# Kernel tuning notes

Hardware: AMD Instinct MI355X
Metric: run time of the kernel (lower is better)

The kernel has to match this reference:

```python
import jax, jax.numpy as jnp
import numpy as np
import math

D_MODEL = 1024
LAYER_ID = 6
NUM_LAYERS = 12
B, T = 8, 2048
MIN_P = -1e38


def _init_params():
    C = D_MODEL
    r01 = LAYER_ID / (NUM_LAYERS - 1)
    r1a0 = 1.0 - LAYER_ID / NUM_LAYERS
    h = np.arange(C, dtype=np.float32)
    decay_speed = -5.0 + 8.0 * (h / (C - 1)) ** (0.7 + 1.3 * r01)
    zigzag = (((np.arange(C) + 1) % 3) - 1).astype(np.float32) * 0.5
    U = np.float32(math.log(0.3)) + zigzag
    xx = (np.arange(C, dtype=np.float32) / C).reshape(1, 1, C)
    tmk = xx ** r1a0
    tmv = xx ** r1a0 + 0.3 * r01
    tmr = xx ** (0.5 * r1a0)
    return (jnp.asarray(decay_speed), jnp.asarray(U), jnp.asarray(tmk, jnp.float32),
            jnp.asarray(tmv, jnp.float32), jnp.asarray(tmr, jnp.float32))


def setup_inputs() -> dict:
    key = jax.random.key(0)
    k0, k1, k2, k3, k4 = jax.random.split(key, 5)
    W, U, tmk, tmv, tmr = _init_params()
    C = D_MODEL
    s = 1.0 / math.sqrt(C)
    return {
        "x": jax.random.normal(k0, (B, T, C), jnp.float32),
        "W": W, "U": U,
        "time_mix_k": tmk, "time_mix_v": tmv, "time_mix_r": tmr,
        "Wk": jax.random.normal(k1, (C, C), jnp.float32) * s,
        "Wv": jax.random.normal(k2, (C, C), jnp.float32) * s,
        "Wr": jax.random.normal(k3, (C, C), jnp.float32) * s,
        "Wo": jax.random.normal(k4, (C, C), jnp.float32) * s,
    }


def _wkv(W, U, k, v):
    # W, U: [C]; k, v: [B, T, C]. Stable WKV recurrence with max-trick.
    w = -jnp.exp(W)  # negative decay, per channel
    Bb, Tt, Cc = k.shape
    aa0 = jnp.zeros((Bb, Cc), k.dtype)
    bb0 = jnp.zeros((Bb, Cc), k.dtype)
    pp0 = jnp.full((Bb, Cc), MIN_P, k.dtype)

    def step(carry, kv_t):
        aa, bb, pp = carry
        kt, vt = kv_t  # [B, C]
        ww = U + kt
        p = jnp.maximum(pp, ww)
        e1 = jnp.exp(pp - p)
        e2 = jnp.exp(ww - p)
        y = (e1 * aa + e2 * vt) / (e1 * bb + e2)
        ww2 = pp + w
        p2 = jnp.maximum(ww2, kt)
        e1b = jnp.exp(ww2 - p2)
        e2b = jnp.exp(kt - p2)
        return (e1b * aa + e2b * vt, e1b * bb + e2b, p2), y

    kT = jnp.swapaxes(k, 0, 1)  # [T, B, C]
    vT = jnp.swapaxes(v, 0, 1)
    _, yT = jax.lax.scan(step, (aa0, bb0, pp0), (kT, vT))
    return jnp.swapaxes(yT, 0, 1)  # [B, T, C]


def reference(x, W, U, time_mix_k, time_mix_v, time_mix_r, Wk, Wv, Wr, Wo):
    # token shift: prepend zero along T, drop last step
    xs = jnp.pad(x, ((0, 0), (1, 0), (0, 0)))[:, :-1]
    xk = x * time_mix_k + xs * (1.0 - time_mix_k)
    xv = x * time_mix_v + xs * (1.0 - time_mix_v)
    xr = x * time_mix_r + xs * (1.0 - time_mix_r)
    K = jnp.einsum('btc,dc->btd', xk, Wk)
    V = jnp.einsum('btc,dc->btd', xv, Wv)
    R = jnp.einsum('btc,dc->btd', xr, Wr)
    wkv = _wkv(W, U, K, V)
    hidden = jax.lax.stop_gradient(wkv[:, -1, :])
    rwkv = jax.nn.sigmoid(R) * wkv
    output = jnp.einsum('btc,dc->btd', rwkv, Wo)
    return output, hidden
```

## Files before the change

kernel.cpp:

```cpp
#include <hip/hip_runtime.h>

#define Bn 8
#define Tn 2048
#define Cn 1024
#define Mn (Bn * Tn)
#define LCH 64
#define NCH (Tn / LCH)

typedef __attribute__((ext_vector_type(8))) short short8;
typedef __attribute__((ext_vector_type(4))) float f32x4;

typedef const __attribute__((address_space(1))) void gas_void;
typedef __attribute__((address_space(3))) void las_void;

__device__ __forceinline__ unsigned short f2bf(float f) {
    unsigned int u = __float_as_uint(f);
    u += 0x7FFFu + ((u >> 16) & 1u);
    return (unsigned short)(u >> 16);
}
__device__ __forceinline__ float bf2f(unsigned short h) {
    return __uint_as_float(((unsigned int)h) << 16);
}

__global__ __launch_bounds__(256) void cvt_kernel(const float* __restrict__ src,
                                                  unsigned short* __restrict__ dst) {
    int i = blockIdx.x * 256 + threadIdx.x;
    float4 v = ((const float4*)src)[i];
    ushort4 o;
    o.x = f2bf(v.x); o.y = f2bf(v.y); o.z = f2bf(v.z); o.w = f2bf(v.w);
    ((ushort4*)dst)[i] = o;
}

__device__ __forceinline__ ushort4 mix4(const float4& a, const float4& s, const float4& m) {
    ushort4 o;
    o.x = f2bf(s.x + (a.x - s.x) * m.x);
    o.y = f2bf(s.y + (a.y - s.y) * m.y);
    o.z = f2bf(s.z + (a.z - s.z) * m.z);
    o.w = f2bf(s.w + (a.w - s.w) * m.w);
    return o;
}

__global__ __launch_bounds__(256) void mix_kernel(const float* __restrict__ x,
                                                  const float* __restrict__ tmk,
                                                  const float* __restrict__ tmv,
                                                  const float* __restrict__ tmr,
                                                  unsigned short* __restrict__ ak,
                                                  unsigned short* __restrict__ av,
                                                  unsigned short* __restrict__ ar) {
    int i = blockIdx.x * 256 + threadIdx.x;
    int c4 = i & 255;
    int t  = (i >> 8) & (Tn - 1);
    float4 xc = ((const float4*)x)[i];
    float4 xs = make_float4(0.f, 0.f, 0.f, 0.f);
    if (t > 0) xs = ((const float4*)x)[i - 256];
    float4 mk = ((const float4*)tmk)[c4];
    float4 mv = ((const float4*)tmv)[c4];
    float4 mr = ((const float4*)tmr)[c4];
    ((ushort4*)ak)[i] = mix4(xc, xs, mk);
    ((ushort4*)av)[i] = mix4(xc, xs, mv);
    ((ushort4*)ar)[i] = mix4(xc, xs, mr);
}

#define BK 32

template <int FOUT>
__global__ __launch_bounds__(256) void gemm_bt(const unsigned short* __restrict__ A,
                                               const unsigned short* __restrict__ Bw,
                                               unsigned short* __restrict__ Cb,
                                               float* __restrict__ Cf) {
    __shared__ unsigned short lA[128 * BK];
    __shared__ unsigned short lB[128 * BK];
    const int tid  = threadIdx.x;
    const int lane = tid & 63;
    const int wid  = tid >> 6;
    const int wr   = wid >> 1;
    const int wc   = wid & 1;
    const int bm   = blockIdx.x * 128;
    const int bn   = blockIdx.y * 128;

    const int srow = lane >> 2;
    const int scol = (lane & 3) * 8;
    const int lr   = lane & 15;
    const int lk   = (lane >> 4) * 8;

    f32x4 acc[4][4] = {};

    for (int k0 = 0; k0 < 1024; k0 += BK) {
#pragma unroll
        for (int i = 0; i < 2; ++i) {
            int r = wid * 32 + i * 16;
            const unsigned short* ga = A  + (size_t)(bm + r + srow) * 1024 + k0 + scol;
            const unsigned short* gb = Bw + (size_t)(bn + r + srow) * 1024 + k0 + scol;
            __builtin_amdgcn_global_load_lds((gas_void*)ga, (las_void*)&lA[r * BK], 16, 0, 0);
            __builtin_amdgcn_global_load_lds((gas_void*)gb, (las_void*)&lB[r * BK], 16, 0, 0);
        }
        __syncthreads();

        short8 af[4], bfv[4];
#pragma unroll
        for (int m = 0; m < 4; ++m)
            af[m] = *(const short8*)&lA[(wr * 64 + m * 16 + lr) * BK + lk];
#pragma unroll
        for (int n = 0; n < 4; ++n)
            bfv[n] = *(const short8*)&lB[(wc * 64 + n * 16 + lr) * BK + lk];
#pragma unroll
        for (int m = 0; m < 4; ++m)
#pragma unroll
            for (int n = 0; n < 4; ++n)
                acc[m][n] = __builtin_amdgcn_mfma_f32_16x16x32_bf16(af[m], bfv[n], acc[m][n], 0, 0, 0);
        __syncthreads();
    }

    const int crow0 = bm + wr * 64 + (lane >> 4) * 4;
    const int ccol0 = bn + wc * 64 + (lane & 15);
#pragma unroll
    for (int m = 0; m < 4; ++m) {
#pragma unroll
        for (int n = 0; n < 4; ++n) {
            int col = ccol0 + n * 16;
#pragma unroll
            for (int j = 0; j < 4; ++j) {
                size_t idx = (size_t)(crow0 + m * 16 + j) * 1024 + col;
                float v = acc[m][n][j];
                if (FOUT) Cf[idx] = v;
                else      Cb[idx] = f2bf(v);
            }
        }
    }
}

__global__ __launch_bounds__(256) void wkv_pass1(const unsigned short* __restrict__ K,
                                                 const unsigned short* __restrict__ V,
                                                 const float* __restrict__ Wd,
                                                 float* __restrict__ caa,
                                                 float* __restrict__ cbb,
                                                 float* __restrict__ cpp) {
    int c = blockIdx.x * 256 + threadIdx.x;
    int j = blockIdx.y;
    int b = blockIdx.z;
    float w = -__expf(Wd[c]);
    float aa = 0.f, bb = 0.f, pp = -1e38f;
    size_t base = ((size_t)(b * Tn + j * LCH)) * Cn + c;
#pragma unroll 4
    for (int t = 0; t < LCH; ++t) {
        size_t idx = base + (size_t)t * Cn;
        float kt = bf2f(K[idx]);
        float vt = bf2f(V[idx]);
        float ww2 = pp + w;
        float p2  = fmaxf(ww2, kt);
        float e1  = __expf(ww2 - p2);
        float e2  = __expf(kt - p2);
        aa = e1 * aa + e2 * vt;
        bb = e1 * bb + e2;
        pp = p2;
    }
    size_t o = ((size_t)b * NCH + j) * Cn + c;
    caa[o] = aa; cbb[o] = bb; cpp[o] = pp;
}

__global__ __launch_bounds__(256) void wkv_pass2(const float* __restrict__ Wd,
                                                 const float* __restrict__ caa,
                                                 const float* __restrict__ cbb,
                                                 const float* __restrict__ cpp,
                                                 float* __restrict__ saa,
                                                 float* __restrict__ sbb,
                                                 float* __restrict__ spp) {
    int c = blockIdx.x * 256 + threadIdx.x;
    int b = blockIdx.y;
    float Lw = -__expf(Wd[c]) * (float)LCH;
    float aa = 0.f, bb = 0.f, pp = -1e38f;
    for (int j = 0; j < NCH; ++j) {
        size_t o = ((size_t)b * NCH + j) * Cn + c;
        saa[o] = aa; sbb[o] = bb; spp[o] = pp;
        float qa = caa[o], qb = cbb[o], qp = cpp[o];
        float ppd = pp + Lw;
        float p  = fmaxf(ppd, qp);
        float e1 = __expf(ppd - p);
        float e2 = __expf(qp - p);
        aa = e1 * aa + e2 * qa;
        bb = e1 * bb + e2 * qb;
        pp = p;
    }
}

__global__ __launch_bounds__(256) void wkv_pass3(const unsigned short* __restrict__ K,
                                                 const unsigned short* __restrict__ V,
                                                 const unsigned short* __restrict__ Rb,
                                                 const float* __restrict__ Wd,
                                                 const float* __restrict__ Ud,
                                                 const float* __restrict__ saa,
                                                 const float* __restrict__ sbb,
                                                 const float* __restrict__ spp,
                                                 unsigned short* __restrict__ rwkv,
                                                 float* __restrict__ hidden) {
    int c = blockIdx.x * 256 + threadIdx.x;
    int j = blockIdx.y;
    int b = blockIdx.z;
    float w = -__expf(Wd[c]);
    float u = Ud[c];
    size_t o = ((size_t)b * NCH + j) * Cn + c;
    float aa = saa[o], bb = sbb[o], pp = spp[o];
    size_t base = ((size_t)(b * Tn + j * LCH)) * Cn + c;
    float y = 0.f;
#pragma unroll 4
    for (int t = 0; t < LCH; ++t) {
        size_t idx = base + (size_t)t * Cn;
        float kt = bf2f(K[idx]);
        float vt = bf2f(V[idx]);
        float rt = bf2f(Rb[idx]);
        float ww = u + kt;
        float p  = fmaxf(pp, ww);
        float e1 = __expf(pp - p);
        float e2 = __expf(ww - p);
        y = __fdividef(e1 * aa + e2 * vt, e1 * bb + e2);
        float sr = __fdividef(1.f, 1.f + __expf(-rt));
        rwkv[idx] = f2bf(sr * y);
        float ww2 = pp + w;
        float p2  = fmaxf(ww2, kt);
        float e1b = __expf(ww2 - p2);
        float e2b = __expf(kt - p2);
        aa = e1b * aa + e2b * vt;
        bb = e1b * bb + e2b;
        pp = p2;
    }
    if (j == NCH - 1) hidden[b * Cn + c] = y;
}

extern "C" void kernel_launch(void* const* d_in, const int* in_sizes, int n_in,
                              void* d_out, int out_size, void* d_ws, size_t ws_size,
                              hipStream_t stream) {
    const float* x   = (const float*)d_in[0];
    const float* Wd  = (const float*)d_in[1];
    const float* Ud  = (const float*)d_in[2];
    const float* tmk = (const float*)d_in[3];
    const float* tmv = (const float*)d_in[4];
    const float* tmr = (const float*)d_in[5];
    const float* Wk  = (const float*)d_in[6];
    const float* Wv  = (const float*)d_in[7];
    const float* Wr  = (const float*)d_in[8];
    const float* Wo  = (const float*)d_in[9];

    float* out    = (float*)d_out;
    float* hidden = out + (size_t)Mn * Cn;

    const size_t MK = (size_t)Mn * Cn;
    const size_t CC = (size_t)Cn * Cn;
    unsigned short* ak  = (unsigned short*)d_ws;
    unsigned short* av  = ak + MK;
    unsigned short* ar  = av + MK;
    unsigned short* Kb  = ar + MK;
    unsigned short* Wkb = Kb + MK;
    unsigned short* Wvb = Wkb + CC;
    unsigned short* Wrb = Wvb + CC;
    unsigned short* Wob = Wrb + CC;
    unsigned short* Vb = ak;
    unsigned short* Rb = av;
    unsigned short* rw = ar;
    const size_t SB = (size_t)Bn * NCH * Cn;
    float* caa = (float*)Wkb;
    float* cbb = caa + SB;
    float* cpp = cbb + SB;
    float* saa = cpp + SB;
    float* sbb = saa + SB;
    float* spp = sbb + SB;

    cvt_kernel<<<dim3(CC / 1024), 256, 0, stream>>>(Wk, Wkb);
    cvt_kernel<<<dim3(CC / 1024), 256, 0, stream>>>(Wv, Wvb);
    cvt_kernel<<<dim3(CC / 1024), 256, 0, stream>>>(Wr, Wrb);
    cvt_kernel<<<dim3(CC / 1024), 256, 0, stream>>>(Wo, Wob);

    mix_kernel<<<dim3(MK / 1024), 256, 0, stream>>>(x, tmk, tmv, tmr, ak, av, ar);

    dim3 gg(Mn / 128, Cn / 128);
    gemm_bt<0><<<gg, 256, 0, stream>>>(ak, Wkb, Kb, nullptr);
    gemm_bt<0><<<gg, 256, 0, stream>>>(av, Wvb, Vb, nullptr);
    gemm_bt<0><<<gg, 256, 0, stream>>>(ar, Wrb, Rb, nullptr);

    dim3 gw(Cn / 256, NCH, Bn);
    wkv_pass1<<<gw, 256, 0, stream>>>(Kb, Vb, Wd, caa, cbb, cpp);
    wkv_pass2<<<dim3(Cn / 256, Bn), 256, 0, stream>>>(Wd, caa, cbb, cpp, saa, sbb, spp);
    wkv_pass3<<<gw, 256, 0, stream>>>(Kb, Vb, Rb, Wd, Ud, saa, sbb, spp, rw, hidden);

    gemm_bt<1><<<gg, 256, 0, stream>>>(rw, Wob, nullptr, out);
}
```

Before: 408.4 us.

## Rewrite bf16 GEMM with 256x128 tiles, triple-buffered LDS and swizzled layout

Replaces the simple single-buffered 128x128 BK=32 GEMM with a 256x128 tile, 512-thread kernel that stages BK=64 slices into a three-deep LDS ring using async global_load_lds, XOR-swizzled rows and split phases with s_setprio around MFMA bursts. The goal is to overlap global loads with MFMA compute, cut LDS bank conflicts and raise reuse per loaded byte across the four GEMMs. It uses 144KB of LDS per block with hand-placed vmcnt waits and raw barriers, which limits occupancy and depends on exact counting of outstanding loads to stay correct.

```diff
diff --git a/kernel.cpp b/kernel.cpp
--- a/kernel.cpp
+++ b/kernel.cpp
@@ -61,67 +61,123 @@
     ((ushort4*)ar)[i] = mix4(xc, xs, mr);
 }
 
-#define BK 32
+
+#define NT 16
+#define BUFB 49152
+
+#define PHASE_BAR() asm volatile("s_barrier" ::: "memory")
+#define WAITV6()    asm volatile("s_waitcnt vmcnt(6)" ::: "memory")
+#define WAITV0()    asm volatile("s_waitcnt vmcnt(0)" ::: "memory")
+
+__device__ __forceinline__ void stage_rows(const unsigned short* gbase,
+                                           char* ldsbase, int lane, int wid) {
+    int rowg = wid * 16 + (lane >> 3);
+    int slot = (lane & 7) ^ (lane >> 3);
+    const unsigned short* s0 = gbase + (size_t)rowg * 1024 + slot * 8;
+    const unsigned short* s1 = gbase + (size_t)(rowg + 8) * 1024 + slot * 8;
+    char* d0 = ldsbase + (wid * 16) * 128;
+    char* d1 = ldsbase + (wid * 16 + 8) * 128;
+    __builtin_amdgcn_global_load_lds((gas_void*)s0, (las_void*)d0, 16, 0, 0);
+    __builtin_amdgcn_global_load_lds((gas_void*)s1, (las_void*)d1, 16, 0, 0);
+}
 
 template <int FOUT>
-__global__ __launch_bounds__(256) void gemm_bt(const unsigned short* __restrict__ A,
-                                               const unsigned short* __restrict__ Bw,
-                                               unsigned short* __restrict__ Cb,
-                                               float* __restrict__ Cf) {
-    __shared__ unsigned short lA[128 * BK];
-    __shared__ unsigned short lB[128 * BK];
+__global__ __launch_bounds__(512, 2) void gemm_bt(const unsigned short* __restrict__ A,
+                                                  const unsigned short* __restrict__ Bw,
+                                                  unsigned short* __restrict__ Cb,
+                                                  float* __restrict__ Cf) {
+    __shared__ char lds[3 * BUFB];
     const int tid  = threadIdx.x;
     const int lane = tid & 63;
     const int wid  = tid >> 6;
-    const int wr   = wid >> 1;
-    const int wc   = wid & 1;
-    const int bm   = blockIdx.x * 128;
+    const int wr   = wid >> 2;
+    const int wc   = wid & 3;
+    const int bm   = blockIdx.x * 256;
     const int bn   = blockIdx.y * 128;
 
-    const int srow = lane >> 2;
-    const int scol = (lane & 3) * 8;
-    const int lr   = lane & 15;
-    const int lk   = (lane >> 4) * 8;
-
-    f32x4 acc[4][4] = {};
-
-    for (int k0 = 0; k0 < 1024; k0 += BK) {
-#pragma unroll
-        for (int i = 0; i < 2; ++i) {
-            int r = wid * 32 + i * 16;
-            const unsigned short* ga = A  + (size_t)(bm + r + srow) * 1024 + k0 + scol;
-            const unsigned short* gb = Bw + (size_t)(bn + r + srow) * 1024 + k0 + scol;
-            __builtin_amdgcn_global_load_lds((gas_void*)ga, (las_void*)&lA[r * BK], 16, 0, 0);
-            __builtin_amdgcn_global_load_lds((gas_void*)gb, (las_void*)&lB[r * BK], 16, 0, 0);
-        }
-        __syncthreads();
-
-        short8 af[4], bfv[4];
-#pragma unroll
-        for (int m = 0; m < 4; ++m)
-            af[m] = *(const short8*)&lA[(wr * 64 + m * 16 + lr) * BK + lk];
-#pragma unroll
-        for (int n = 0; n < 4; ++n)
-            bfv[n] = *(const short8*)&lB[(wc * 64 + n * 16 + lr) * BK + lk];
-#pragma unroll
-        for (int m = 0; m < 4; ++m)
-#pragma unroll
-            for (int n = 0; n < 4; ++n)
-                acc[m][n] = __builtin_amdgcn_mfma_f32_16x16x32_bf16(af[m], bfv[n], acc[m][n], 0, 0, 0);
-        __syncthreads();
-    }
-
-    const int crow0 = bm + wr * 64 + (lane >> 4) * 4;
-    const int ccol0 = bn + wc * 64 + (lane & 15);
-#pragma unroll
-    for (int m = 0; m < 4; ++m) {
-#pragma unroll
-        for (int n = 0; n < 4; ++n) {
-            int col = ccol0 + n * 16;
+    const int lr = lane & 15;
+    const int q  = lane >> 4;
+    const int s7 = lr & 7;
+
+    f32x4 acc[8][2] = {};
+
+    stage_rows(A  + (size_t)bm * 1024,                 lds,                 lane, wid);
+    stage_rows(A  + (size_t)(bm + 128) * 1024,         lds + 16384,         lane, wid);
+    stage_rows(Bw + (size_t)bn * 1024,                 lds + 32768,         lane, wid);
+    stage_rows(A  + (size_t)bm * 1024 + 64,            lds + BUFB,          lane, wid);
+    stage_rows(A  + (size_t)(bm + 128) * 1024 + 64,    lds + BUFB + 16384,  lane, wid);
+    stage_rows(Bw + (size_t)bn * 1024 + 64,            lds + BUFB + 32768,  lane, wid);
+    WAITV6();
+    PHASE_BAR();
+
+    int cur = 0, nxt2 = 2;
+#pragma unroll 1
+    for (int t = 0; t < NT; ++t) {
+        char* Ab = lds + cur * BUFB;
+        char* Bb = Ab + 32768;
+        const bool st = (t + 2) < NT;
+        char* An = lds + nxt2 * BUFB;
+        const unsigned short* gA = A  + (size_t)bm * 1024 + (t + 2) * 64;
+        const unsigned short* gB = Bw + (size_t)bn * 1024 + (t + 2) * 64;
+
+        short8 af[8], bf0, bf1;
+        if (st) stage_rows(gA, An, lane, wid);
+#pragma unroll
+        for (int mi = 0; mi < 8; ++mi)
+            af[mi] = *(const short8*)(Ab + (wr * 128 + mi * 16 + lr) * 128 + ((q ^ s7) << 4));
+        bf0 = *(const short8*)(Bb + (wc * 32 + lr) * 128 + ((q ^ s7) << 4));
+        __builtin_amdgcn_s_setprio(1);
+#pragma unroll
+        for (int mi = 0; mi < 8; ++mi)
+            acc[mi][0] = __builtin_amdgcn_mfma_f32_16x16x32_bf16(af[mi], bf0, acc[mi][0], 0, 0, 0);
+        __builtin_amdgcn_s_setprio(0);
+        PHASE_BAR();
+
+        if (st) stage_rows(gA + (size_t)128 * 1024, An + 16384, lane, wid);
+        bf1 = *(const short8*)(Bb + (wc * 32 + 16 + lr) * 128 + ((q ^ s7) << 4));
+        __builtin_amdgcn_s_setprio(1);
+#pragma unroll
+        for (int mi = 0; mi < 8; ++mi)
+            acc[mi][1] = __builtin_amdgcn_mfma_f32_16x16x32_bf16(af[mi], bf1, acc[mi][1], 0, 0, 0);
+        __builtin_amdgcn_s_setprio(0);
+        PHASE_BAR();
+
+        if (st) stage_rows(gB, An + 32768, lane, wid);
+#pragma unroll
+        for (int mi = 0; mi < 8; ++mi)
+            af[mi] = *(const short8*)(Ab + (wr * 128 + mi * 16 + lr) * 128 + (((q | 4) ^ s7) << 4));
+        bf0 = *(const short8*)(Bb + (wc * 32 + lr) * 128 + (((q | 4) ^ s7) << 4));
+        __builtin_amdgcn_s_setprio(1);
+#pragma unroll
+        for (int mi = 0; mi < 8; ++mi)
+            acc[mi][0] = __builtin_amdgcn_mfma_f32_16x16x32_bf16(af[mi], bf0, acc[mi][0], 0, 0, 0);
+        __builtin_amdgcn_s_setprio(0);
+        PHASE_BAR();
+
+        bf1 = *(const short8*)(Bb + (wc * 32 + 16 + lr) * 128 + (((q | 4) ^ s7) << 4));
+        __builtin_amdgcn_s_setprio(1);
+#pragma unroll
+        for (int mi = 0; mi < 8; ++mi)
+            acc[mi][1] = __builtin_amdgcn_mfma_f32_16x16x32_bf16(af[mi], bf1, acc[mi][1], 0, 0, 0);
+        __builtin_amdgcn_s_setprio(0);
+        if (t <= NT - 3) { WAITV6(); } else { WAITV0(); }
+        PHASE_BAR();
+
+        cur  = (cur  == 2) ? 0 : cur + 1;
+        nxt2 = (nxt2 == 2) ? 0 : nxt2 + 1;
+    }
+
+    const int crow0 = bm + wr * 128 + q * 4;
+    const int ccol0 = bn + wc * 32 + lr;
+#pragma unroll
+    for (int mi = 0; mi < 8; ++mi) {
+#pragma unroll
+        for (int ni = 0; ni < 2; ++ni) {
+            int col = ccol0 + ni * 16;
 #pragma unroll
             for (int j = 0; j < 4; ++j) {
-                size_t idx = (size_t)(crow0 + m * 16 + j) * 1024 + col;
-                float v = acc[m][n][j];
+                size_t idx = (size_t)(crow0 + mi * 16 + j) * 1024 + col;
+                float v = acc[mi][ni][j];
                 if (FOUT) Cf[idx] = v;
                 else      Cb[idx] = f2bf(v);
             }
@@ -271,15 +327,15 @@
 
     mix_kernel<<<dim3(MK / 1024), 256, 0, stream>>>(x, tmk, tmv, tmr, ak, av, ar);
 
-    dim3 gg(Mn / 128, Cn / 128);
-    gemm_bt<0><<<gg, 256, 0, stream>>>(ak, Wkb, Kb, nullptr);
-    gemm_bt<0><<<gg, 256, 0, stream>>>(av, Wvb, Vb, nullptr);
-    gemm_bt<0><<<gg, 256, 0, stream>>>(ar, Wrb, Rb, nullptr);
+    dim3 gg(Mn / 256, Cn / 128);
+    gemm_bt<0><<<gg, 512, 0, stream>>>(ak, Wkb, Kb, nullptr);
+    gemm_bt<0><<<gg, 512, 0, stream>>>(av, Wvb, Vb, nullptr);
+    gemm_bt<0><<<gg, 512, 0, stream>>>(ar, Wrb, Rb, nullptr);
 
     dim3 gw(Cn / 256, NCH, Bn);
     wkv_pass1<<<gw, 256, 0, stream>>>(Kb, Vb, Wd, caa, cbb, cpp);
     wkv_pass2<<<dim3(Cn / 256, Bn), 256, 0, stream>>>(Wd, caa, cbb, cpp, saa, sbb, spp);
     wkv_pass3<<<gw, 256, 0, stream>>>(Kb, Vb, Rb, Wd, Ud, saa, sbb, spp, rw, hidden);
 
-    gemm_bt<1><<<gg, 256, 0, stream>>>(rw, Wob, nullptr, out);
-}
+    gemm_bt<1><<<gg, 512, 0, stream>>>(rw, Wob, nullptr, out);
+}
```

Measured after the change: 383.9 us. 1.06x faster.
